# Kernel tuning notes

Measured on AMD Instinct MI355X. Metric: run time of the kernel, lower is better.

The kernel has to match this reference:

```python
import jax, jax.numpy as jnp
import numpy as np

B, D, H = 1024, 64, 128


def setup_inputs() -> dict:
    key = jax.random.key(0)
    ks = jax.random.split(key, 12)
    s1 = 1.0 / np.sqrt(4 * D)
    sh = 1.0 / np.sqrt(H)
    sd = 1.0 / np.sqrt(D)
    return {
        "x": jax.random.normal(ks[0], (B, D), dtype=jnp.float32),
        # edge_fn: Linear(4D,H) -> ReLU -> Linear(H,H)
        "W1": jax.random.uniform(ks[1], (4 * D, H), minval=-s1, maxval=s1, dtype=jnp.float32),
        "b1": jax.random.uniform(ks[2], (H,), minval=-s1, maxval=s1, dtype=jnp.float32),
        "W2": jax.random.uniform(ks[3], (H, H), minval=-sh, maxval=sh, dtype=jnp.float32),
        "b2": jax.random.uniform(ks[4], (H,), minval=-sh, maxval=sh, dtype=jnp.float32),
        # tau_proj: Linear(D,1) -> Softplus
        "Wt": jax.random.uniform(ks[5], (D, 1), minval=-sd, maxval=sd, dtype=jnp.float32),
        "bt": jax.random.uniform(ks[6], (1,), minval=-sd, maxval=sd, dtype=jnp.float32),
        # agg: Linear(H,H) -> ReLU
        "Wa": jax.random.uniform(ks[7], (H, H), minval=-sh, maxval=sh, dtype=jnp.float32),
        "ba": jax.random.uniform(ks[8], (H,), minval=-sh, maxval=sh, dtype=jnp.float32),
        # res_proj: Linear(D,H)
        "Wr": jax.random.uniform(ks[9], (D, H), minval=-sd, maxval=sd, dtype=jnp.float32),
        "br": jax.random.uniform(ks[10], (H,), minval=-sd, maxval=sd, dtype=jnp.float32),
        # LayerNorm(H)
        "gamma": jnp.ones((H,), dtype=jnp.float32),
        "beta": jnp.zeros((H,), dtype=jnp.float32),
    }


def reference(x, W1, b1, W2, b2, Wt, bt, Wa, ba, Wr, br, gamma, beta):
    d = x.shape[1]
    # Decompose first linear over concat([x_i, x_j, delta, |delta|]) into 4 sub-matmuls;
    # only the |delta| term needs the pairwise [B,B,D] tensor.
    Wi, Wj, Wd, Wab = W1[:d], W1[d:2 * d], W1[2 * d:3 * d], W1[3 * d:]
    ti = x @ Wi            # [B,H] (i-dependent)
    tj = x @ Wj            # [B,H] (j-dependent)
    td = x @ Wd            # [B,H] (delta = x_i - x_j contribution)
    delta = x[:, None, :] - x[None, :, :]             # [B,B,D]
    ta = jnp.einsum('ijd,dh->ijh', jnp.abs(delta), Wab)  # [B,B,H]
    pre = ti[:, None, :] + tj[None, :, :] + td[:, None, :] - td[None, :, :] + ta + b1
    d_proj = jax.nn.relu(pre) @ W2 + b2               # [B,B,H]
    tau = jnp.maximum(jax.nn.softplus(x @ Wt + bt), 0.01) + 1.0  # [B,1]
    h_mean = d_proj.mean(axis=1) / tau                # mean over j
    h = jax.nn.relu(h_mean @ Wa + ba)
    y = h + (x @ Wr + br)
    mu = y.mean(axis=-1, keepdims=True)
    var = ((y - mu) ** 2).mean(axis=-1, keepdims=True)  # biased, like torch LayerNorm
    return (y - mu) * jax.lax.rsqrt(var + 1e-5) * gamma + beta
```

## Files before the change

### kernel.cpp

```cpp
#include <hip/hip_runtime.h>
#include <hip/hip_bf16.h>
#include <math.h>

#define BB 1024
#define DD 64
#define HH 128

typedef __bf16 bf16x8 __attribute__((ext_vector_type(8)));
typedef float floatx4 __attribute__((ext_vector_type(4)));

__device__ __forceinline__ unsigned short f2bf(float v) {
    union { float f; unsigned u; } a; a.f = v;
    unsigned r = a.u + 0x7fffu + ((a.u >> 16) & 1u);
    return (unsigned short)(r >> 16);
}

__device__ __forceinline__ void async_cp16(const float* g, float* lds_wave_base) {
    __builtin_amdgcn_global_load_lds(
        (const __attribute__((address_space(1))) unsigned int*)g,
        (__attribute__((address_space(3))) unsigned int*)lds_wave_base,
        16, 0, 0);
}

__global__ __launch_bounds__(256) void prep_kernel(
    const float* __restrict__ x, const float* __restrict__ W1,
    const float* __restrict__ b1,
    float* __restrict__ c1, float* __restrict__ c2P,
    unsigned short* __restrict__ wpack)
{
    __shared__ float xr[2][DD];
    const int t = threadIdx.x;
    const int i0 = blockIdx.x * 2;
    if (t < 2 * DD) xr[t >> 6][t & 63] = x[i0 * DD + t];
    __syncthreads();

    const int ii = t >> 7, h = t & 127;
    const int i = i0 + ii;
    float a1 = 0.f, a2 = 0.f;
    #pragma unroll 16
    for (int k = 0; k < DD; k++) {
        float wi = W1[k * HH + h];
        float wj = W1[(DD + k) * HH + h];
        float wd = W1[(2 * DD + k) * HH + h];
        float xv = xr[ii][k];
        a1 = fmaf(xv, wi + wd, a1);
        a2 = fmaf(xv, wj - wd, a2);
    }
    c1[i * HH + h] = a1 + b1[h];
    const int jl = i & 15;
    c2P[(i >> 4) * 2048 + (h >> 4) * 256 + (((jl >> 2) << 4) | (h & 15)) * 4 + (jl & 3)] = a2;

    if (blockIdx.x < 64) {
        int f = blockIdx.x * 256 + t;
        int jj = f & 7, l = (f >> 3) & 63, u = f >> 9;
        int s = u & 1, t8 = u >> 1;
        int k = s * 32 + ((l >> 4) << 3) + jj;
        int hh = t8 * 16 + (l & 15);
        wpack[f] = f2bf(W1[(3 * DD + k) * HH + hh]);
    }
}

__global__ __launch_bounds__(256) void pair_kernel(
    const float* __restrict__ x, const float* __restrict__ c1,
    const float* __restrict__ c2P, const unsigned short* __restrict__ wpack,
    float* __restrict__ Sp)
{
    __shared__ __align__(16) float xs[2][1024];

    const int t = threadIdx.x;
    const int wave = t >> 6;
    const int l = t & 63;
    const int quad = l >> 4, lm = l & 15;
    const int ig = blockIdx.x >> 2;
    const int jq = blockIdx.x & 3;
    const int i = ig * 4 + wave;
    const int j0base = jq * 256;
    const int sw = lm & 7;

    async_cp16(x + (j0base + (t >> 4)) * DD + (((t & 15) ^ ((t >> 4) & 7)) << 2),
               &xs[0][0] + wave * 256);

    float xi[16];
    {
        const float* xg = x + i * DD + quad * 8;
        *(float4*)(xi)      = *(const float4*)(xg);
        *(float4*)(xi + 4)  = *(const float4*)(xg + 4);
        *(float4*)(xi + 8)  = *(const float4*)(xg + 32);
        *(float4*)(xi + 12) = *(const float4*)(xg + 36);
    }
    float c1r[8];
    #pragma unroll
    for (int t8 = 0; t8 < 8; t8++) c1r[t8] = c1[i * HH + t8 * 16 + lm];
    bf16x8 wf[16];
    #pragma unroll
    for (int u = 0; u < 16; u++)
        wf[u] = *(const bf16x8*)(wpack + (u * 64 + l) * 8);

    float S[8];
    #pragma unroll
    for (int t8 = 0; t8 < 8; t8++) S[t8] = 0.f;

    for (int tile = 0; tile < 16; ++tile) {
        const int cur = tile & 1;
        __syncthreads();

        if (tile < 15) {
            const int jn = j0base + (tile + 1) * 16;
            async_cp16(x + (jn + (t >> 4)) * DD + (((t & 15) ^ ((t >> 4) & 7)) << 2),
                       &xs[cur ^ 1][0] + wave * 256);
        }

        const float* cg = c2P + ((j0base + tile * 16) >> 4) * 2048;
        floatx4 acc[8];
        #pragma unroll
        for (int t8 = 0; t8 < 8; t8++) {
            float4 c2v = *(const float4*)(cg + t8 * 256 + l * 4);
            acc[t8][0] = c2v.x + c1r[t8];
            acc[t8][1] = c2v.y + c1r[t8];
            acc[t8][2] = c2v.z + c1r[t8];
            acc[t8][3] = c2v.w + c1r[t8];
        }

        const float* xb = &xs[cur][lm * 64];
        float4 a0 = *(const float4*)(xb + (((quad * 2)     ^ sw) << 2));
        float4 a1 = *(const float4*)(xb + (((quad * 2 + 1) ^ sw) << 2));
        float4 a2 = *(const float4*)(xb + (((quad * 2 + 8) ^ sw) << 2));
        float4 a3 = *(const float4*)(xb + (((quad * 2 + 9) ^ sw) << 2));
        bf16x8 af0, af1;
        af0[0] = (__bf16)fabsf(xi[0] - a0.x);  af0[1] = (__bf16)fabsf(xi[1] - a0.y);
        af0[2] = (__bf16)fabsf(xi[2] - a0.z);  af0[3] = (__bf16)fabsf(xi[3] - a0.w);
        af0[4] = (__bf16)fabsf(xi[4] - a1.x);  af0[5] = (__bf16)fabsf(xi[5] - a1.y);
        af0[6] = (__bf16)fabsf(xi[6] - a1.z);  af0[7] = (__bf16)fabsf(xi[7] - a1.w);
        af1[0] = (__bf16)fabsf(xi[8] - a2.x);  af1[1] = (__bf16)fabsf(xi[9] - a2.y);
        af1[2] = (__bf16)fabsf(xi[10] - a2.z); af1[3] = (__bf16)fabsf(xi[11] - a2.w);
        af1[4] = (__bf16)fabsf(xi[12] - a3.x); af1[5] = (__bf16)fabsf(xi[13] - a3.y);
        af1[6] = (__bf16)fabsf(xi[14] - a3.z); af1[7] = (__bf16)fabsf(xi[15] - a3.w);

        #pragma unroll
        for (int t8 = 0; t8 < 8; t8++) {
            acc[t8] = __builtin_amdgcn_mfma_f32_16x16x32_bf16(af0, wf[t8 * 2 + 0], acc[t8], 0, 0, 0);
            acc[t8] = __builtin_amdgcn_mfma_f32_16x16x32_bf16(af1, wf[t8 * 2 + 1], acc[t8], 0, 0, 0);
        }
        #pragma unroll
        for (int t8 = 0; t8 < 8; t8++) {
            S[t8] += fmaxf(acc[t8][0], 0.f);
            S[t8] += fmaxf(acc[t8][1], 0.f);
            S[t8] += fmaxf(acc[t8][2], 0.f);
            S[t8] += fmaxf(acc[t8][3], 0.f);
        }
    }

    #pragma unroll
    for (int t8 = 0; t8 < 8; t8++) {
        S[t8] += __shfl_xor(S[t8], 16, 64);
        S[t8] += __shfl_xor(S[t8], 32, 64);
    }
    if (quad == 0) {
        #pragma unroll
        for (int t8 = 0; t8 < 8; t8++)
            Sp[(jq * BB + i) * HH + t8 * 16 + lm] = S[t8];
    }
}

__global__ __launch_bounds__(256) void finish_kernel(
    const float* __restrict__ Sp, const float* __restrict__ W2,
    const float* __restrict__ b2, const float* __restrict__ x,
    const float* __restrict__ Wt, const float* __restrict__ bt,
    const float* __restrict__ Wa, const float* __restrict__ ba,
    const float* __restrict__ Wr, const float* __restrict__ br,
    const float* __restrict__ gamma, const float* __restrict__ beta,
    float* __restrict__ out)
{
    __shared__ float Srow[2][HH];
    __shared__ float mrow[2][HH];
    __shared__ float xrow[2][DD];
    __shared__ float taus[2];
    __shared__ float red1[2][2];
    __shared__ float red2[2][2];
    const int t = threadIdx.x;
    const int ii = t >> 7, h = t & 127;
    const int i = blockIdx.x * 2 + ii;

    float s = 0.f;
    #pragma unroll
    for (int q = 0; q < 4; q++) s += Sp[(q * BB + i) * HH + h];
    Srow[ii][h] = s * (1.0f / (float)BB);
    if (h < 64) xrow[ii][h] = x[i * DD + h];

    if ((t & 127) < 64) {
        int lane = t & 63;
        float p = x[i * DD + lane] * Wt[lane];
        #pragma unroll
        for (int off = 32; off; off >>= 1) p += __shfl_down(p, off, 64);
        if (lane == 0) {
            float z = p + bt[0];
            float sp = (z > 20.f) ? z : log1pf(expf(z));
            taus[ii] = fmaxf(sp, 0.01f) + 1.0f;
        }
    }
    __syncthreads();

    float acc = b2[h];
    #pragma unroll 8
    for (int k = 0; k < HH; k++) acc += Srow[ii][k] * W2[k * HH + h];
    float mv = acc / taus[ii];
    mrow[ii][h] = mv;
    __syncthreads();

    float acc2 = ba[h];
    #pragma unroll 8
    for (int k = 0; k < HH; k++) acc2 += mrow[ii][k] * Wa[k * HH + h];
    float y = fmaxf(acc2, 0.f) + br[h];
    #pragma unroll 8
    for (int d = 0; d < DD; d++) y += xrow[ii][d] * Wr[d * HH + h];

    const int wv = (t >> 6) & 1;
    const int lane = t & 63;
    float p = y;
    #pragma unroll
    for (int off = 32; off; off >>= 1) p += __shfl_down(p, off, 64);
    if (lane == 0) red1[ii][wv] = p;
    __syncthreads();
    float mu = (red1[ii][0] + red1[ii][1]) * (1.f / (float)HH);
    float dy = y - mu;
    float q = dy * dy;
    #pragma unroll
    for (int off = 32; off; off >>= 1) q += __shfl_down(q, off, 64);
    if (lane == 0) red2[ii][wv] = q;
    __syncthreads();
    float var = (red2[ii][0] + red2[ii][1]) * (1.f / (float)HH);
    out[i * HH + h] = dy * rsqrtf(var + 1e-5f) * gamma[h] + beta[h];
}

extern "C" void kernel_launch(void* const* d_in, const int* in_sizes, int n_in,
                              void* d_out, int out_size, void* d_ws, size_t ws_size,
                              hipStream_t stream)
{
    const float* x     = (const float*)d_in[0];
    const float* W1    = (const float*)d_in[1];
    const float* b1    = (const float*)d_in[2];
    const float* W2    = (const float*)d_in[3];
    const float* b2    = (const float*)d_in[4];
    const float* Wt    = (const float*)d_in[5];
    const float* bt    = (const float*)d_in[6];
    const float* Wa    = (const float*)d_in[7];
    const float* ba    = (const float*)d_in[8];
    const float* Wr    = (const float*)d_in[9];
    const float* br    = (const float*)d_in[10];
    const float* gamma = (const float*)d_in[11];
    const float* beta  = (const float*)d_in[12];
    float* out = (float*)d_out;

    char* ws = (char*)d_ws;
    float*          c1    = (float*)(ws);
    float*          c2P   = (float*)(ws + (512 << 10));
    unsigned short* wpack = (unsigned short*)(ws + (1024 << 10));
    float*          Sp    = (float*)(ws + (1056 << 10));

    prep_kernel<<<512, 256, 0, stream>>>(x, W1, b1, c1, c2P, wpack);
    pair_kernel<<<1024, 256, 0, stream>>>(x, c1, c2P, wpack, Sp);
    finish_kernel<<<BB / 2, 256, 0, stream>>>(Sp, W2, b2, x, Wt, bt,
                                              Wa, ba, Wr, br, gamma, beta, out);
}
```

Baseline: 141.5 us.

## Stage c2 tiles through LDS asynchronously and vectorize prep/finish kernels

The pair kernel now prefetches each tile's c2P slice into a double-buffered LDS array using async global-to-LDS copies, alongside the existing x tile prefetch. This replaces direct global loads inside the compute loop. The prep and finish kernels now process 8 rows per block with float4 weight loads and 32-lane shuffle reductions. That cuts the number of blocks and replaces LDS-based LayerNorm reductions with in-register xor shuffles. The costs are 16KB of extra LDS per pair block and fewer blocks in the small kernels, which leaves fewer workgroups than CUs.

```diff
diff --git a/kernel.cpp b/kernel.cpp
--- a/kernel.cpp
+++ b/kernel.cpp
@@ -28,27 +28,46 @@
     float* __restrict__ c1, float* __restrict__ c2P,
     unsigned short* __restrict__ wpack)
 {
-    __shared__ float xr[2][DD];
+    __shared__ float xs[8][DD];
     const int t = threadIdx.x;
-    const int i0 = blockIdx.x * 2;
-    if (t < 2 * DD) xr[t >> 6][t & 63] = x[i0 * DD + t];
+    const int i0 = blockIdx.x * 8;
+    xs[t >> 6][t & 63] = x[i0 * DD + t];
+    xs[4 + (t >> 6)][t & 63] = x[i0 * DD + 256 + t];
     __syncthreads();
 
-    const int ii = t >> 7, h = t & 127;
+    const int ii = t >> 5;
+    const int h4 = t & 31;
+    const int h = h4 * 4;
     const int i = i0 + ii;
-    float a1 = 0.f, a2 = 0.f;
-    #pragma unroll 16
+
+    float4 a1 = {0.f, 0.f, 0.f, 0.f};
+    float4 a2 = {0.f, 0.f, 0.f, 0.f};
+    #pragma unroll 4
     for (int k = 0; k < DD; k++) {
-        float wi = W1[k * HH + h];
-        float wj = W1[(DD + k) * HH + h];
-        float wd = W1[(2 * DD + k) * HH + h];
-        float xv = xr[ii][k];
-        a1 = fmaf(xv, wi + wd, a1);
-        a2 = fmaf(xv, wj - wd, a2);
-    }
-    c1[i * HH + h] = a1 + b1[h];
+        float4 wi = *(const float4*)(W1 + k * HH + h);
+        float4 wj = *(const float4*)(W1 + (DD + k) * HH + h);
+        float4 wd = *(const float4*)(W1 + (2 * DD + k) * HH + h);
+        float xv = xs[ii][k];
+        a1.x = fmaf(xv, wi.x + wd.x, a1.x);
+        a1.y = fmaf(xv, wi.y + wd.y, a1.y);
+        a1.z = fmaf(xv, wi.z + wd.z, a1.z);
+        a1.w = fmaf(xv, wi.w + wd.w, a1.w);
+        a2.x = fmaf(xv, wj.x - wd.x, a2.x);
+        a2.y = fmaf(xv, wj.y - wd.y, a2.y);
+        a2.z = fmaf(xv, wj.z - wd.z, a2.z);
+        a2.w = fmaf(xv, wj.w - wd.w, a2.w);
+    }
+    float4 b1v = *(const float4*)(b1 + h);
+    float4 c1v = {a1.x + b1v.x, a1.y + b1v.y, a1.z + b1v.z, a1.w + b1v.w};
+    *(float4*)(c1 + i * HH + h) = c1v;
+
     const int jl = i & 15;
-    c2P[(i >> 4) * 2048 + (h >> 4) * 256 + (((jl >> 2) << 4) | (h & 15)) * 4 + (jl & 3)] = a2;
+    float* cb = c2P + (i >> 4) * 2048 + (h >> 4) * 256 + (jl & 3);
+    const int p0 = ((jl >> 2) * 16 + (h & 15));
+    cb[(p0 + 0) * 4] = a2.x;
+    cb[(p0 + 1) * 4] = a2.y;
+    cb[(p0 + 2) * 4] = a2.z;
+    cb[(p0 + 3) * 4] = a2.w;
 
     if (blockIdx.x < 64) {
         int f = blockIdx.x * 256 + t;
@@ -66,6 +85,7 @@
     float* __restrict__ Sp)
 {
     __shared__ __align__(16) float xs[2][1024];
+    __shared__ __align__(16) float c2s[2][2048];
 
     const int t = threadIdx.x;
     const int wave = t >> 6;
@@ -79,6 +99,11 @@
 
     async_cp16(x + (j0base + (t >> 4)) * DD + (((t & 15) ^ ((t >> 4) & 7)) << 2),
                &xs[0][0] + wave * 256);
+    {
+        const float* cg = c2P + (j0base >> 4) * 2048;
+        async_cp16(cg + t * 4,        &c2s[0][0]    + wave * 256);
+        async_cp16(cg + 1024 + t * 4, &c2s[0][1024] + wave * 256);
+    }
 
     float xi[16];
     {
@@ -108,13 +133,15 @@
             const int jn = j0base + (tile + 1) * 16;
             async_cp16(x + (jn + (t >> 4)) * DD + (((t & 15) ^ ((t >> 4) & 7)) << 2),
                        &xs[cur ^ 1][0] + wave * 256);
-        }
-
-        const float* cg = c2P + ((j0base + tile * 16) >> 4) * 2048;
+            const float* cg = c2P + (jn >> 4) * 2048;
+            async_cp16(cg + t * 4,        &c2s[cur ^ 1][0]    + wave * 256);
+            async_cp16(cg + 1024 + t * 4, &c2s[cur ^ 1][1024] + wave * 256);
+        }
+
         floatx4 acc[8];
         #pragma unroll
         for (int t8 = 0; t8 < 8; t8++) {
-            float4 c2v = *(const float4*)(cg + t8 * 256 + l * 4);
+            float4 c2v = *(const float4*)(&c2s[cur][t8 * 256 + l * 4]);
             acc[t8][0] = c2v.x + c1r[t8];
             acc[t8][1] = c2v.y + c1r[t8];
             acc[t8][2] = c2v.z + c1r[t8];
@@ -171,28 +198,36 @@
     const float* __restrict__ gamma, const float* __restrict__ beta,
     float* __restrict__ out)
 {
-    __shared__ float Srow[2][HH];
-    __shared__ float mrow[2][HH];
-    __shared__ float xrow[2][DD];
-    __shared__ float taus[2];
-    __shared__ float red1[2][2];
-    __shared__ float red2[2][2];
+    __shared__ float Srow[8][HH];
+    __shared__ float mrow[8][HH];
+    __shared__ float xrow[8][DD];
+    __shared__ float taus[8];
     const int t = threadIdx.x;
-    const int ii = t >> 7, h = t & 127;
-    const int i = blockIdx.x * 2 + ii;
-
-    float s = 0.f;
-    #pragma unroll
-    for (int q = 0; q < 4; q++) s += Sp[(q * BB + i) * HH + h];
-    Srow[ii][h] = s * (1.0f / (float)BB);
-    if (h < 64) xrow[ii][h] = x[i * DD + h];
-
-    if ((t & 127) < 64) {
-        int lane = t & 63;
-        float p = x[i * DD + lane] * Wt[lane];
-        #pragma unroll
-        for (int off = 32; off; off >>= 1) p += __shfl_down(p, off, 64);
-        if (lane == 0) {
+    const int ii = t >> 5;
+    const int h4 = t & 31;
+    const int h = h4 * 4;
+    const int i0 = blockIdx.x * 8;
+    const int i = i0 + ii;
+
+    {
+        float4 s = {0.f, 0.f, 0.f, 0.f};
+        #pragma unroll
+        for (int q = 0; q < 4; q++) {
+            float4 v = *(const float4*)(Sp + (q * BB + i) * HH + h);
+            s.x += v.x; s.y += v.y; s.z += v.z; s.w += v.w;
+        }
+        const float inv = 1.0f / (float)BB;
+        float4 sm = {s.x * inv, s.y * inv, s.z * inv, s.w * inv};
+        *(float4*)(&Srow[ii][h]) = sm;
+    }
+    xrow[t >> 6][t & 63] = x[i0 * DD + t];
+    xrow[4 + (t >> 6)][t & 63] = x[i0 * DD + 256 + t];
+
+    {
+        float p = x[i * DD + h4] * Wt[h4] + x[i * DD + 32 + h4] * Wt[32 + h4];
+        #pragma unroll
+        for (int off = 16; off; off >>= 1) p += __shfl_xor(p, off, 64);
+        if (h4 == 0) {
             float z = p + bt[0];
             float sp = (z > 20.f) ? z : log1pf(expf(z));
             taus[ii] = fmaxf(sp, 0.01f) + 1.0f;
@@ -200,36 +235,52 @@
     }
     __syncthreads();
 
-    float acc = b2[h];
+    float4 acc = *(const float4*)(b2 + h);
     #pragma unroll 8
-    for (int k = 0; k < HH; k++) acc += Srow[ii][k] * W2[k * HH + h];
-    float mv = acc / taus[ii];
-    mrow[ii][h] = mv;
+    for (int k = 0; k < HH; k++) {
+        float4 w = *(const float4*)(W2 + k * HH + h);
+        float sv = Srow[ii][k];
+        acc.x = fmaf(sv, w.x, acc.x); acc.y = fmaf(sv, w.y, acc.y);
+        acc.z = fmaf(sv, w.z, acc.z); acc.w = fmaf(sv, w.w, acc.w);
+    }
+    const float itau = 1.0f / taus[ii];
+    float4 mv = {acc.x * itau, acc.y * itau, acc.z * itau, acc.w * itau};
+    *(float4*)(&mrow[ii][h]) = mv;
     __syncthreads();
 
-    float acc2 = ba[h];
+    float4 a2 = *(const float4*)(ba + h);
     #pragma unroll 8
-    for (int k = 0; k < HH; k++) acc2 += mrow[ii][k] * Wa[k * HH + h];
-    float y = fmaxf(acc2, 0.f) + br[h];
+    for (int k = 0; k < HH; k++) {
+        float4 w = *(const float4*)(Wa + k * HH + h);
+        float sv = mrow[ii][k];
+        a2.x = fmaf(sv, w.x, a2.x); a2.y = fmaf(sv, w.y, a2.y);
+        a2.z = fmaf(sv, w.z, a2.z); a2.w = fmaf(sv, w.w, a2.w);
+    }
+    float4 brv = *(const float4*)(br + h);
+    float4 y = {fmaxf(a2.x, 0.f) + brv.x, fmaxf(a2.y, 0.f) + brv.y,
+                fmaxf(a2.z, 0.f) + brv.z, fmaxf(a2.w, 0.f) + brv.w};
     #pragma unroll 8
-    for (int d = 0; d < DD; d++) y += xrow[ii][d] * Wr[d * HH + h];
-
-    const int wv = (t >> 6) & 1;
-    const int lane = t & 63;
-    float p = y;
-    #pragma unroll
-    for (int off = 32; off; off >>= 1) p += __shfl_down(p, off, 64);
-    if (lane == 0) red1[ii][wv] = p;
-    __syncthreads();
-    float mu = (red1[ii][0] + red1[ii][1]) * (1.f / (float)HH);
-    float dy = y - mu;
-    float q = dy * dy;
-    #pragma unroll
-    for (int off = 32; off; off >>= 1) q += __shfl_down(q, off, 64);
-    if (lane == 0) red2[ii][wv] = q;
-    __syncthreads();
-    float var = (red2[ii][0] + red2[ii][1]) * (1.f / (float)HH);
-    out[i * HH + h] = dy * rsqrtf(var + 1e-5f) * gamma[h] + beta[h];
+    for (int d = 0; d < DD; d++) {
+        float4 w = *(const float4*)(Wr + d * HH + h);
+        float xv = xrow[ii][d];
+        y.x = fmaf(xv, w.x, y.x); y.y = fmaf(xv, w.y, y.y);
+        y.z = fmaf(xv, w.z, y.z); y.w = fmaf(xv, w.w, y.w);
+    }
+
+    float p = y.x + y.y + y.z + y.w;
+    #pragma unroll
+    for (int off = 16; off; off >>= 1) p += __shfl_xor(p, off, 64);
+    float mu = p * (1.0f / (float)HH);
+    float4 dy = {y.x - mu, y.y - mu, y.z - mu, y.w - mu};
+    float q = dy.x * dy.x + dy.y * dy.y + dy.z * dy.z + dy.w * dy.w;
+    #pragma unroll
+    for (int off = 16; off; off >>= 1) q += __shfl_xor(q, off, 64);
+    float rs = rsqrtf(q * (1.0f / (float)HH) + 1e-5f);
+    float4 gv = *(const float4*)(gamma + h);
+    float4 bv = *(const float4*)(beta + h);
+    float4 o = {dy.x * rs * gv.x + bv.x, dy.y * rs * gv.y + bv.y,
+                dy.z * rs * gv.z + bv.z, dy.w * rs * gv.w + bv.w};
+    *(float4*)(out + i * HH + h) = o;
 }
 
 extern "C" void kernel_launch(void* const* d_in, const int* in_sizes, int n_in,
@@ -257,8 +308,8 @@
     unsigned short* wpack = (unsigned short*)(ws + (1024 << 10));
     float*          Sp    = (float*)(ws + (1056 << 10));
 
-    prep_kernel<<<512, 256, 0, stream>>>(x, W1, b1, c1, c2P, wpack);
+    prep_kernel<<<128, 256, 0, stream>>>(x, W1, b1, c1, c2P, wpack);
     pair_kernel<<<1024, 256, 0, stream>>>(x, c1, c2P, wpack, Sp);
-    finish_kernel<<<BB / 2, 256, 0, stream>>>(Sp, W2, b2, x, Wt, bt,
-                                              Wa, ba, Wr, br, gamma, beta, out);
-}
+    finish_kernel<<<128, 256, 0, stream>>>(Sp, W2, b2, x, Wt, bt,
+                                           Wa, ba, Wr, br, gamma, beta, out);
+}
```

After: 147.8 us. +4.5%, slower.
